# Performance work log

Measured on AMD Instinct MI355X. Metric: run time of the kernel, lower is better.

The kernel has to match this reference:

```python
import jax, jax.numpy as jnp
import numpy as np

B, N, D, DEPTH = 1, 512, 128, 4


def mlp_apply(W, x):
    # W: (depth, d, d), x: (..., d). First layer has no activation, then silu before each matmul.
    x = x @ W[0]
    for i in range(1, DEPTH):
        x = jax.nn.silu(x) @ W[i]
    return x


def _binop(x, y):
    # linear recurrence combine: s_t = a_t * s_{t-1} + b_t
    a1, b1 = x
    a2, b2 = y
    return (a1 * a2, a2 * b1 + b2)


def setup_inputs() -> dict:
    key = jax.random.key(0)
    ks = jax.random.split(key, 7)
    s = 0.02  # scale for projection weights (torch Linear-like init magnitude)
    return {
        "seq": jax.random.normal(ks[0], (B, N, D), jnp.float32),
        "W_mem": jax.random.normal(ks[1], (DEPTH, D, D), jnp.float32) * (D ** -0.5),
        "W_q": jax.random.normal(ks[2], (D, D), jnp.float32) * s,
        "W_kv": jax.random.normal(ks[3], (D, 2 * D), jnp.float32) * s,
        "W_mom": jax.random.normal(ks[4], (D, 1), jnp.float32) * s,
        "W_step": jax.random.normal(ks[5], (D, 1), jnp.float32) * s,
        "W_decay": jax.random.normal(ks[6], (D, 1), jnp.float32) * s,
    }


def reference(seq, W_mem, W_q, W_kv, W_mom, W_step, W_decay):
    b, n, d = seq.shape
    # --- store_memories ---
    adaptive_lr = (seq @ W_step)[..., 0]            # (b, n)
    adaptive_mom = seq @ W_mom                      # (b, n, 1)
    decay = jax.nn.sigmoid(seq @ W_decay)           # (b, n, 1)

    kv = seq.reshape(b * n, d) @ W_kv               # (bn, 2d)
    keys, values = kv[:, :d], kv[:, d:]

    def loss_fn(W, k, v):
        pred = mlp_apply(W, k)                      # (d,)
        # (pred - v)^2 .mean(-1).sum() for a single sample == mean over d
        return jnp.mean((pred - v) ** 2)

    # per-sample meta-gradients wrt memory MLP weights
    losses, grads = jax.vmap(jax.value_and_grad(loss_fn, argnums=0), in_axes=(None, 0, 0))(W_mem, keys, values)
    grads = grads.reshape(b, n, DEPTH, d, d)
    surprise = grads * (-adaptive_lr)[..., None, None, None]   # (b,n,depth,d,d)

    # momentum_t = adaptive_mom_t * momentum_{t-1} + surprise_t  (assoc. scan over n)
    am = adaptive_mom[..., None, None]              # (b, n, 1, 1, 1)
    _, momentum = jax.lax.associative_scan(_binop, (am, surprise), axis=1)

    # update_t = (1 - decay_t) * update_{t-1} + momentum_t
    dec = (1.0 - decay)[..., None, None]            # (b, n, 1, 1, 1)
    _, updates = jax.lax.associative_scan(_binop, (dec, momentum), axis=1)

    # --- retrieve_memories with per-token updated weights ---
    q = (seq @ W_q).reshape(b * n, d)
    W_tok = (W_mem[None, None] + updates).reshape(b * n, DEPTH, d, d)
    retrieved = jax.vmap(mlp_apply)(W_tok, q).reshape(b, n, d)
    return retrieved
```

## Files before the change

### kernel.cpp

```cpp
#include <hip/hip_runtime.h>
#include <hip/hip_bf16.h>
#include <math.h>

#define N 512
#define NN (N*N)
#define D 128
#define DD (D*D)
#define ND (N*D)
#define LSTR 132
#define CSTR 68

__device__ __forceinline__ float sigmoidf_(float x) { return 1.f / (1.f + expf(-x)); }

__global__ void k_transpose(const float* __restrict__ W_mem, float* __restrict__ WT) {
    int idx = blockIdx.x * 256 + threadIdx.x;
    int l = idx / DD;
    int r = idx % DD;
    int i = r / D;
    int j = r % D;
    WT[idx] = W_mem[(l + 1) * DD + j * D + i];
}

__global__ __launch_bounds__(512) void k_phase1(
    const float* __restrict__ seq, const float* __restrict__ W_mem,
    const float* __restrict__ W_q, const float* __restrict__ W_kv,
    const float* __restrict__ W_mom, const float* __restrict__ W_step,
    const float* __restrict__ W_decay, const float* __restrict__ WT,
    float* __restrict__ Q, float* __restrict__ INS, float* __restrict__ ES,
    float* __restrict__ am, float* __restrict__ dec)
{
    __shared__ float s_seq[2][D];
    __shared__ float s_bufA[2][D];
    __shared__ float s_bufB[2][D];
    __shared__ float s_p3[4][2][3][D];
    __shared__ float s_part[4][2][D];
    __shared__ float s_red8[8][3];
    __shared__ float s_lr[2];

    const int tid = threadIdx.x;
    const int p   = tid >> 7;
    const int j   = tid & 127;
    const int t0  = blockIdx.x * 2;
    const int i0  = p * 32;

    if (p < 2) s_seq[p][j] = seq[(t0 + p) * D + j];
    __syncthreads();

    {
        const int wv   = tid >> 6;
        const int tok  = wv >> 2;
        const int half = (wv >> 1) & 1;
        float sv = s_seq[tok][j];
        float p0 = 0.f, p1 = 0.f, p2 = 0.f;
        if (half == 0) { p0 = sv * W_step[j]; p1 = sv * W_mom[j]; }
        else           { p2 = sv * W_decay[j]; }
#pragma unroll
        for (int off = 32; off > 0; off >>= 1) {
            p0 += __shfl_down(p0, off);
            p1 += __shfl_down(p1, off);
            p2 += __shfl_down(p2, off);
        }
        if ((tid & 63) == 0) {
            s_red8[wv][0] = p0; s_red8[wv][1] = p1; s_red8[wv][2] = p2;
        }
    }
    __syncthreads();
    if (tid < 2) {
        int b = tid * 4;
        s_lr[tid]  = s_red8[b][0] + s_red8[b + 1][0];
        am[t0+tid] = s_red8[b][1] + s_red8[b + 1][1];
        dec[t0+tid]= 1.f - sigmoidf_(s_red8[b + 2][2] + s_red8[b + 3][2]);
    }

    float k0 = 0.f, v0 = 0.f, q0 = 0.f;
    float k1 = 0.f, v1 = 0.f, q1 = 0.f;
#pragma unroll 8
    for (int ii = 0; ii < 32; ii++) {
        int i = i0 + ii;
        float wk = W_kv[i * 256 + j];
        float wq = W_q[i * 128 + j];
        float wvv = W_kv[i * 256 + 128 + j];
        float a0 = s_seq[0][i], a1 = s_seq[1][i];
        k0 += a0 * wk;  k1 += a1 * wk;
        v0 += a0 * wvv; v1 += a1 * wvv;
        q0 += a0 * wq;  q1 += a1 * wq;
    }
    s_p3[p][0][0][j] = k0; s_p3[p][0][1][j] = v0; s_p3[p][0][2][j] = q0;
    s_p3[p][1][0][j] = k1; s_p3[p][1][1][j] = v1; s_p3[p][1][2][j] = q1;
    __syncthreads();

    float vj = 0.f;
    if (p < 2) {
        const int tok = p;
        float kj = s_p3[0][tok][0][j] + s_p3[1][tok][0][j] + s_p3[2][tok][0][j] + s_p3[3][tok][0][j];
        vj       = s_p3[0][tok][1][j] + s_p3[1][tok][1][j] + s_p3[2][tok][1][j] + s_p3[3][tok][1][j];
        float qj = s_p3[0][tok][2][j] + s_p3[1][tok][2][j] + s_p3[2][tok][2][j] + s_p3[3][tok][2][j];
        Q[(t0 + tok) * D + j] = qj;
        INS[(t0 + tok) * D + j] = kj;
        s_bufA[tok][j] = kj;
    }
    __syncthreads();

    float hreg[4];
    float pred = 0.f;
    {
        float (*bufs[2])[D] = { s_bufA, s_bufB };
        for (int l = 0; l < 4; l++) {
            float (*cur)[D] = bufs[l & 1];
            float (*nxt)[D] = bufs[(l + 1) & 1];
            const float* Wp = W_mem + l * DD + j;
            float a0 = 0.f, a1 = 0.f;
#pragma unroll 8
            for (int ii = 0; ii < 32; ii++) {
                int i = i0 + ii;
                float w = Wp[i * D];
                a0 += cur[0][i] * w;
                a1 += cur[1][i] * w;
            }
            s_part[p][0][j] = a0;
            s_part[p][1][j] = a1;
            __syncthreads();
            if (p < 2) {
                const int tok = p;
                float y = (s_part[0][tok][j] + s_part[1][tok][j])
                        + (s_part[2][tok][j] + s_part[3][tok][j]);
                hreg[l] = y;
                if (l < 3) {
                    float a = y * sigmoidf_(y);
                    nxt[tok][j] = a;
                    INS[(l + 1) * ND + (t0 + tok) * D + j] = a;
                } else {
                    pred = y;
                }
            }
            __syncthreads();
        }

        if (p < 2) {
            const int tok = p;
            float e = -s_lr[tok] * (2.f / (float)D) * (pred - vj);
            ES[3 * ND + (t0 + tok) * D + j] = e;
            bufs[0][tok][j] = e;
        }
        __syncthreads();

        for (int l = 3; l >= 1; l--) {
            float (*cur)[D] = bufs[(3 - l) & 1];
            float (*nxt)[D] = bufs[(3 - l + 1) & 1];
            const float* Wp = WT + (l - 1) * DD + j;
            float a0 = 0.f, a1 = 0.f;
#pragma unroll 8
            for (int ii = 0; ii < 32; ii++) {
                int i = i0 + ii;
                float w = Wp[i * D];
                a0 += cur[0][i] * w;
                a1 += cur[1][i] * w;
            }
            s_part[p][0][j] = a0;
            s_part[p][1][j] = a1;
            __syncthreads();
            if (p < 2) {
                const int tok = p;
                float g = (s_part[0][tok][j] + s_part[1][tok][j])
                        + (s_part[2][tok][j] + s_part[3][tok][j]);
                float h = hreg[l - 1];
                float sg = sigmoidf_(h);
                float e2 = g * (sg * (1.f + h * (1.f - sg)));
                ES[(l - 1) * ND + (t0 + tok) * D + j] = e2;
                nxt[tok][j] = e2;
            }
            __syncthreads();
        }
    }
}

__global__ __launch_bounds__(512) void k_logscan(
    const float* __restrict__ am, const float* __restrict__ dec,
    double* __restrict__ LA, double* __restrict__ LDp, int* __restrict__ NC)
{
    __shared__ double sa[N], sd[N];
    __shared__ int sn[N];
    const int t = threadIdx.x;
    float a = am[t];
    float d = dec[t];
    sa[t] = log((double)fmaxf(fabsf(a), 1e-38f));
    sd[t] = log((double)fmaxf(d, 1e-38f));
    sn[t] = (a < 0.f) ? 1 : 0;
    __syncthreads();
    for (int off = 1; off < N; off <<= 1) {
        double va = 0.0, vd = 0.0; int vn = 0;
        if (t >= off) { va = sa[t - off]; vd = sd[t - off]; vn = sn[t - off]; }
        __syncthreads();
        sa[t] += va; sd[t] += vd; sn[t] += vn;
        __syncthreads();
    }
    LA[t] = sa[t]; LDp[t] = sd[t]; NC[t] = sn[t];
}

__global__ __launch_bounds__(256) void k_build(
    const double* __restrict__ LA, const double* __restrict__ LDp,
    const int* __restrict__ NC,
    float* __restrict__ Amat, float* __restrict__ Dmat)
{
    int idx = blockIdx.x * 256 + threadIdx.x;
    int u = idx >> 9;
    int s = idx & (N - 1);
    float va = 0.f, vd = 0.f;
    if (s <= u) {
        va = expf((float)(LA[u] - LA[s]));
        if ((NC[u] - NC[s]) & 1) va = -va;
        vd = expf((float)(LDp[u] - LDp[s]));
    }
    Amat[idx] = va;
    Dmat[idx] = vd;
}

__global__ __launch_bounds__(256) void k_betamm(
    const float* __restrict__ Dmat, const float* __restrict__ Amat,
    float* __restrict__ betaP)
{
    const int bs = blockIdx.x;
    const int bt = blockIdx.y;
    const int z  = blockIdx.z;
    if (bs > bt) return;
    const int span = bt - bs + 1;
    const int chunk = (span + 3) >> 2;
    const int kBeg = bs + z * chunk;
    const int kEnd = (kBeg + chunk < bt + 1) ? (kBeg + chunk) : (bt + 1);
    if (kBeg >= kEnd) return;

    __shared__ float sA[32 * 34];
    __shared__ float sDT[32 * 34];

    const int tid = threadIdx.x;
    const int tx = tid & 15;
    const int ty = tid >> 4;
    float acc00 = 0.f, acc01 = 0.f, acc10 = 0.f, acc11 = 0.f;

    for (int kt = kBeg; kt < kEnd; kt++) {
        for (int i = tid; i < 1024; i += 256) {
            int r = i >> 5, c = i & 31;
            sA[r * 34 + c]  = Amat[(kt * 32 + r) * N + bs * 32 + c];
            sDT[c * 34 + r] = Dmat[(bt * 32 + r) * N + kt * 32 + c];
        }
        __syncthreads();
#pragma unroll 8
        for (int k = 0; k < 32; k++) {
            float2 a = *(float2*)&sA[k * 34 + 2 * tx];
            float2 d = *(float2*)&sDT[k * 34 + 2 * ty];
            acc00 += d.x * a.x; acc01 += d.x * a.y;
            acc10 += d.y * a.x; acc11 += d.y * a.y;
        }
        __syncthreads();
    }
    float* bp = betaP + z * NN + (bt * 32 + 2 * ty) * N + bs * 32 + 2 * tx;
    *(float2*)bp       = make_float2(acc00, acc01);
    *(float2*)(bp + N) = make_float2(acc10, acc11);
}

__global__ __launch_bounds__(256) void k_betared(
    const float* __restrict__ betaP, float* __restrict__ beta)
{
    int idx4 = blockIdx.x * 256 + threadIdx.x;
    int t  = idx4 >> 7;
    int s0 = (idx4 & 127) * 4;
    int bt = t >> 5, bs = s0 >> 5;
    float4 v = make_float4(0.f, 0.f, 0.f, 0.f);
    if (bs <= bt) {
        int span = bt - bs + 1;
        int chunk = (span + 3) >> 2;
        int nz = (span + chunk - 1) / chunk;
        v = *(const float4*)(betaP + t * N + s0);
        for (int z = 1; z < nz; z++) {
            float4 u = *(const float4*)(betaP + z * NN + t * N + s0);
            v.x += u.x; v.y += u.y; v.z += u.z; v.w += u.w;
        }
    }
    *(float4*)(beta + t * N + s0) = v;
}

__global__ __launch_bounds__(256) void k_layer(
    const float* __restrict__ Xsrc, float* __restrict__ Pout,
    const float* __restrict__ Wl, const float* __restrict__ INSl,
    const float* __restrict__ ESl, const float* __restrict__ beta,
    int mode)
{
    const int r = blockIdx.x;
    const int z = blockIdx.y;
    const bool isW = (z == 8);
    if (!isW && 4 * z > r) return;
    const int t0 = r * 16;
    const int lane = threadIdx.x;

    __shared__ __align__(16) float sX[16 * LSTR];
    __shared__ __align__(16) float sI[64 * LSTR];
    __shared__ __align__(16) float sE[32 * LSTR];
    __shared__ __align__(16) float sc[16 * CSTR];

    const int nzs = (r >> 2) + 1;
#pragma unroll
    for (int i = 0; i < 2; i++) {
        int f4 = lane + 256 * i;
        int row = f4 >> 5, c4 = f4 & 31;
        float4 v = ((const float4*)(Xsrc + t0 * D))[f4];
        if (mode) {
            for (int zz = 1; zz < nzs; zz++) {
                float4 u = ((const float4*)(Xsrc + zz * ND + t0 * D))[f4];
                v.x += u.x; v.y += u.y; v.z += u.z; v.w += u.w;
            }
            float4 w = ((const float4*)(Xsrc + 8 * ND + t0 * D))[f4];
            v.x += w.x; v.y += w.y; v.z += w.z; v.w += w.w;
            v.x = v.x * sigmoidf_(v.x); v.y = v.y * sigmoidf_(v.y);
            v.z = v.z * sigmoidf_(v.z); v.w = v.w * sigmoidf_(v.w);
        }
        *(float4*)(sX + row * LSTR + c4 * 4) = v;
    }

    if (isW) {
        __syncthreads();
        const int ti  = lane >> 4;
        const int j8  = (lane & 15) * 8;
        float acc[8];
#pragma unroll
        for (int b = 0; b < 8; b++) acc[b] = 0.f;
#pragma unroll 4
        for (int k = 0; k < D; k++) {
            float4 w0 = *(const float4*)(Wl + k * D + j8);
            float4 w1 = *(const float4*)(Wl + k * D + j8 + 4);
            float xv = sX[ti * LSTR + k];
            acc[0] += xv * w0.x; acc[1] += xv * w0.y;
            acc[2] += xv * w0.z; acc[3] += xv * w0.w;
            acc[4] += xv * w1.x; acc[5] += xv * w1.y;
            acc[6] += xv * w1.z; acc[7] += xv * w1.w;
        }
        float* yp = Pout + 8 * ND + (t0 + ti) * D + j8;
        *(float4*)yp       = make_float4(acc[0], acc[1], acc[2], acc[3]);
        *(float4*)(yp + 4) = make_float4(acc[4], acc[5], acc[6], acc[7]);
        return;
    }

    const int s0 = z * 64;
#pragma unroll
    for (int i = 0; i < 8; i++) {
        int f4 = lane + 256 * i;
        int row = f4 >> 5, c4 = f4 & 31;
        float4 a = ((const float4*)(INSl + s0 * D))[f4];
        *(float4*)(sI + row * LSTR + c4 * 4) = a;
    }

    const int rp = lane >> 5;
    const int sp = lane & 31;
    float b00 = beta[(t0 + 2 * rp) * N + s0 + sp];
    float b01 = beta[(t0 + 2 * rp) * N + s0 + sp + 32];
    float b10 = beta[(t0 + 2 * rp + 1) * N + s0 + sp];
    float b11 = beta[(t0 + 2 * rp + 1) * N + s0 + sp + 32];
    __syncthreads();

    float g00 = 0.f, g01 = 0.f, g10 = 0.f, g11 = 0.f;
#pragma unroll 8
    for (int k4 = 0; k4 < D; k4 += 4) {
        float4 a0 = *(float4*)(sX + (2 * rp) * LSTR + k4);
        float4 a1 = *(float4*)(sX + (2 * rp + 1) * LSTR + k4);
        float4 p0 = *(float4*)(sI + sp * LSTR + k4);
        float4 p1 = *(float4*)(sI + (sp + 32) * LSTR + k4);
        g00 += a0.x * p0.x + a0.y * p0.y + a0.z * p0.z + a0.w * p0.w;
        g01 += a0.x * p1.x + a0.y * p1.y + a0.z * p1.z + a0.w * p1.w;
        g10 += a1.x * p0.x + a1.y * p0.y + a1.z * p0.z + a1.w * p0.w;
        g11 += a1.x * p1.x + a1.y * p1.y + a1.z * p1.z + a1.w * p1.w;
    }
    sc[(2 * rp) * CSTR + sp]          = g00 * b00;
    sc[(2 * rp) * CSTR + sp + 32]     = g01 * b01;
    sc[(2 * rp + 1) * CSTR + sp]      = g10 * b10;
    sc[(2 * rp + 1) * CSTR + sp + 32] = g11 * b11;

    const int tp = lane >> 5;
    const int jc = (lane & 31) * 4;
    float acc[2][4];
#pragma unroll
    for (int a = 0; a < 2; a++)
#pragma unroll
        for (int b = 0; b < 4; b++) acc[a][b] = 0.f;

    for (int sub = 0; sub < 2; sub++) {
        __syncthreads();
#pragma unroll
        for (int i = 0; i < 4; i++) {
            int f4 = lane + 256 * i;
            int row = f4 >> 5, c4 = f4 & 31;
            float4 b = ((const float4*)(ESl + (s0 + sub * 32) * D))[f4];
            *(float4*)(sE + row * LSTR + c4 * 4) = b;
        }
        __syncthreads();
        const float* scp0 = sc + tp * CSTR + sub * 32;
        const float* scp1 = sc + (tp + 8) * CSTR + sub * 32;
#pragma unroll 8
        for (int s = 0; s < 32; s++) {
            float c0 = scp0[s];
            float c1 = scp1[s];
            float4 e = *(float4*)(sE + s * LSTR + jc);
            acc[0][0] += c0 * e.x; acc[0][1] += c0 * e.y;
            acc[0][2] += c0 * e.z; acc[0][3] += c0 * e.w;
            acc[1][0] += c1 * e.x; acc[1][1] += c1 * e.y;
            acc[1][2] += c1 * e.z; acc[1][3] += c1 * e.w;
        }
    }

    float* yp0 = Pout + z * ND + (t0 + tp) * D + jc;
    float* yp1 = Pout + z * ND + (t0 + tp + 8) * D + jc;
    *(float4*)yp0 = make_float4(acc[0][0], acc[0][1], acc[0][2], acc[0][3]);
    *(float4*)yp1 = make_float4(acc[1][0], acc[1][1], acc[1][2], acc[1][3]);
}

__global__ __launch_bounds__(256) void k_reduce(
    const float* __restrict__ P, float* __restrict__ out)
{
    int f4 = blockIdx.x * 256 + threadIdx.x;
    int t = f4 >> 5;
    int r = t >> 4;
    int nzs = (r >> 2) + 1;
    float4 v = ((const float4*)P)[f4];
    for (int zz = 1; zz < nzs; zz++) {
        float4 u = ((const float4*)(P + zz * ND))[f4];
        v.x += u.x; v.y += u.y; v.z += u.z; v.w += u.w;
    }
    float4 w = ((const float4*)(P + 8 * ND))[f4];
    v.x += w.x; v.y += w.y; v.z += w.z; v.w += w.w;
    ((float4*)out)[f4] = v;
}

extern "C" void kernel_launch(void* const* d_in, const int* in_sizes, int n_in,
                              void* d_out, int out_size, void* d_ws, size_t ws_size,
                              hipStream_t stream) {
    const float* seq     = (const float*)d_in[0];
    const float* W_mem   = (const float*)d_in[1];
    const float* W_q     = (const float*)d_in[2];
    const float* W_kv    = (const float*)d_in[3];
    const float* W_mom   = (const float*)d_in[4];
    const float* W_step  = (const float*)d_in[5];
    const float* W_decay = (const float*)d_in[6];
    float* out = (float*)d_out;

    float* ws   = (float*)d_ws;
    float* am   = ws;
    float* dec  = am + N;
    float* Q    = dec + N;
    float* INS  = Q + ND;
    float* ES   = INS + 4 * ND;
    float* beta = ES + 4 * ND;
    float* WT   = beta + NN;
    float* Amat = WT + 3 * DD;
    float* Dmat = Amat + NN;
    float* Pa   = Dmat + NN;
    float* Pb   = Pa + 9 * ND;
    double* LA  = (double*)(Pb + 9 * ND);
    double* LDp = LA + N;
    int* NC     = (int*)(LDp + N);
    float* betaP = Pa;

    k_transpose<<<192, 256, 0, stream>>>(W_mem, WT);
    k_phase1<<<N / 2, 512, 0, stream>>>(seq, W_mem, W_q, W_kv, W_mom, W_step, W_decay,
                                        WT, Q, INS, ES, am, dec);
    k_logscan<<<1, N, 0, stream>>>(am, dec, LA, LDp, NC);
    k_build<<<(NN) / 256, 256, 0, stream>>>(LA, LDp, NC, Amat, Dmat);
    dim3 mmgrid(N / 32, N / 32, 4);
    k_betamm<<<mmgrid, 256, 0, stream>>>(Dmat, Amat, betaP);
    k_betared<<<NN / 4 / 256, 256, 0, stream>>>(betaP, beta);

    dim3 lgrid(32, 9);
    k_layer<<<lgrid, 256, 0, stream>>>(Q,  Pa, W_mem,          INS,          ES,          beta, 0);
    k_layer<<<lgrid, 256, 0, stream>>>(Pa, Pb, W_mem + DD,     INS + ND,     ES + ND,     beta, 1);
    k_layer<<<lgrid, 256, 0, stream>>>(Pb, Pa, W_mem + 2 * DD, INS + 2 * ND, ES + 2 * ND, beta, 1);
    k_layer<<<lgrid, 256, 0, stream>>>(Pa, Pb, W_mem + 3 * DD, INS + 3 * ND, ES + 3 * ND, beta, 1);
    k_reduce<<<64, 256, 0, stream>>>(Pb, out);
}
```

Before: 163.5 us.

## Fuse decay-matrix construction into beta matmul and fold split-K reduction into layers

Removes the k_build kernel by computing the A and D decay-matrix tiles on the fly inside k_betamm from the log-scan prefix sums. It also removes the k_betared kernel: each k_layer reads the split-K partials directly and sums them per element. Partials now get their own workspace region so they survive across the layer kernels. This saves two launches and the NN-sized intermediate writes and reads. In exchange, expf is recomputed per tile load and each layer does repeated strided partial reads, four times over.

```diff
diff --git a/kernel.cpp b/kernel.cpp
--- a/kernel.cpp
+++ b/kernel.cpp
@@ -197,27 +197,9 @@
     LA[t] = sa[t]; LDp[t] = sd[t]; NC[t] = sn[t];
 }
 
-__global__ __launch_bounds__(256) void k_build(
+__global__ __launch_bounds__(256) void k_betamm(
     const double* __restrict__ LA, const double* __restrict__ LDp,
-    const int* __restrict__ NC,
-    float* __restrict__ Amat, float* __restrict__ Dmat)
-{
-    int idx = blockIdx.x * 256 + threadIdx.x;
-    int u = idx >> 9;
-    int s = idx & (N - 1);
-    float va = 0.f, vd = 0.f;
-    if (s <= u) {
-        va = expf((float)(LA[u] - LA[s]));
-        if ((NC[u] - NC[s]) & 1) va = -va;
-        vd = expf((float)(LDp[u] - LDp[s]));
-    }
-    Amat[idx] = va;
-    Dmat[idx] = vd;
-}
-
-__global__ __launch_bounds__(256) void k_betamm(
-    const float* __restrict__ Dmat, const float* __restrict__ Amat,
-    float* __restrict__ betaP)
+    const int* __restrict__ NC, float* __restrict__ betaP)
 {
     const int bs = blockIdx.x;
     const int bt = blockIdx.y;
@@ -240,8 +222,15 @@
     for (int kt = kBeg; kt < kEnd; kt++) {
         for (int i = tid; i < 1024; i += 256) {
             int r = i >> 5, c = i & 31;
-            sA[r * 34 + c]  = Amat[(kt * 32 + r) * N + bs * 32 + c];
-            sDT[c * 34 + r] = Dmat[(bt * 32 + r) * N + kt * 32 + c];
+            int u2 = kt * 32 + r, s2 = bs * 32 + c;
+            float va = 0.f;
+            if (s2 <= u2) {
+                va = expf((float)(LA[u2] - LA[s2]));
+                if ((NC[u2] - NC[s2]) & 1) va = -va;
+            }
+            sA[r * 34 + c] = va;
+            int u1 = bt * 32 + r, s1 = kt * 32 + c;
+            sDT[c * 34 + r] = (s1 <= u1) ? expf((float)(LDp[u1] - LDp[s1])) : 0.f;
         }
         __syncthreads();
 #pragma unroll 8
@@ -258,31 +247,21 @@
     *(float2*)(bp + N) = make_float2(acc10, acc11);
 }
 
-__global__ __launch_bounds__(256) void k_betared(
-    const float* __restrict__ betaP, float* __restrict__ beta)
-{
-    int idx4 = blockIdx.x * 256 + threadIdx.x;
-    int t  = idx4 >> 7;
-    int s0 = (idx4 & 127) * 4;
-    int bt = t >> 5, bs = s0 >> 5;
-    float4 v = make_float4(0.f, 0.f, 0.f, 0.f);
-    if (bs <= bt) {
-        int span = bt - bs + 1;
-        int chunk = (span + 3) >> 2;
-        int nz = (span + chunk - 1) / chunk;
-        v = *(const float4*)(betaP + t * N + s0);
-        for (int z = 1; z < nz; z++) {
-            float4 u = *(const float4*)(betaP + z * NN + t * N + s0);
-            v.x += u.x; v.y += u.y; v.z += u.z; v.w += u.w;
-        }
-    }
-    *(float4*)(beta + t * N + s0) = v;
+__device__ __forceinline__ float beta_at(const float* __restrict__ betaP, int t, int s) {
+    int bt = t >> 5, bs = s >> 5;
+    if (bs > bt) return 0.f;
+    int span = bt - bs + 1;
+    int chunk = (span + 3) >> 2;
+    int nz = (span + chunk - 1) / chunk;
+    float v = betaP[t * N + s];
+    for (int z = 1; z < nz; z++) v += betaP[z * NN + t * N + s];
+    return v;
 }
 
 __global__ __launch_bounds__(256) void k_layer(
     const float* __restrict__ Xsrc, float* __restrict__ Pout,
     const float* __restrict__ Wl, const float* __restrict__ INSl,
-    const float* __restrict__ ESl, const float* __restrict__ beta,
+    const float* __restrict__ ESl, const float* __restrict__ betaP,
     int mode)
 {
     const int r = blockIdx.x;
@@ -350,10 +329,10 @@
 
     const int rp = lane >> 5;
     const int sp = lane & 31;
-    float b00 = beta[(t0 + 2 * rp) * N + s0 + sp];
-    float b01 = beta[(t0 + 2 * rp) * N + s0 + sp + 32];
-    float b10 = beta[(t0 + 2 * rp + 1) * N + s0 + sp];
-    float b11 = beta[(t0 + 2 * rp + 1) * N + s0 + sp + 32];
+    float b00 = beta_at(betaP, t0 + 2 * rp,     s0 + sp);
+    float b01 = beta_at(betaP, t0 + 2 * rp,     s0 + sp + 32);
+    float b10 = beta_at(betaP, t0 + 2 * rp + 1, s0 + sp);
+    float b11 = beta_at(betaP, t0 + 2 * rp + 1, s0 + sp + 32);
     __syncthreads();
 
     float g00 = 0.f, g01 = 0.f, g10 = 0.f, g11 = 0.f;
@@ -440,36 +419,31 @@
     const float* W_decay = (const float*)d_in[6];
     float* out = (float*)d_out;
 
-    float* ws   = (float*)d_ws;
-    float* am   = ws;
-    float* dec  = am + N;
-    float* Q    = dec + N;
-    float* INS  = Q + ND;
-    float* ES   = INS + 4 * ND;
-    float* beta = ES + 4 * ND;
-    float* WT   = beta + NN;
-    float* Amat = WT + 3 * DD;
-    float* Dmat = Amat + NN;
-    float* Pa   = Dmat + NN;
-    float* Pb   = Pa + 9 * ND;
-    double* LA  = (double*)(Pb + 9 * ND);
-    double* LDp = LA + N;
-    int* NC     = (int*)(LDp + N);
-    float* betaP = Pa;
+    float* ws    = (float*)d_ws;
+    float* am    = ws;
+    float* dec   = am + N;
+    float* Q     = dec + N;
+    float* INS   = Q + ND;
+    float* ES    = INS + 4 * ND;
+    float* betaP = ES + 4 * ND;
+    float* Pa    = betaP + 4 * NN;
+    float* Pb    = Pa + 9 * ND;
+    float* WT    = Pb + 9 * ND;
+    double* LA   = (double*)(WT + 3 * DD);
+    double* LDp  = LA + N;
+    int* NC      = (int*)(LDp + N);
 
     k_transpose<<<192, 256, 0, stream>>>(W_mem, WT);
     k_phase1<<<N / 2, 512, 0, stream>>>(seq, W_mem, W_q, W_kv, W_mom, W_step, W_decay,
                                         WT, Q, INS, ES, am, dec);
     k_logscan<<<1, N, 0, stream>>>(am, dec, LA, LDp, NC);
-    k_build<<<(NN) / 256, 256, 0, stream>>>(LA, LDp, NC, Amat, Dmat);
     dim3 mmgrid(N / 32, N / 32, 4);
-    k_betamm<<<mmgrid, 256, 0, stream>>>(Dmat, Amat, betaP);
-    k_betared<<<NN / 4 / 256, 256, 0, stream>>>(betaP, beta);
+    k_betamm<<<mmgrid, 256, 0, stream>>>(LA, LDp, NC, betaP);
 
     dim3 lgrid(32, 9);
-    k_layer<<<lgrid, 256, 0, stream>>>(Q,  Pa, W_mem,          INS,          ES,          beta, 0);
-    k_layer<<<lgrid, 256, 0, stream>>>(Pa, Pb, W_mem + DD,     INS + ND,     ES + ND,     beta, 1);
-    k_layer<<<lgrid, 256, 0, stream>>>(Pb, Pa, W_mem + 2 * DD, INS + 2 * ND, ES + 2 * ND, beta, 1);
-    k_layer<<<lgrid, 256, 0, stream>>>(Pa, Pb, W_mem + 3 * DD, INS + 3 * ND, ES + 3 * ND, beta, 1);
+    k_layer<<<lgrid, 256, 0, stream>>>(Q,  Pa, W_mem,          INS,          ES,          betaP, 0);
+    k_layer<<<lgrid, 256, 0, stream>>>(Pa, Pb, W_mem + DD,     INS + ND,     ES + ND,     betaP, 1);
+    k_layer<<<lgrid, 256, 0, stream>>>(Pb, Pa, W_mem + 2 * DD, INS + 2 * ND, ES + 2 * ND, betaP, 1);
+    k_layer<<<lgrid, 256, 0, stream>>>(Pa, Pb, W_mem + 3 * DD, INS + 3 * ND, ES + 3 * ND, betaP, 1);
     k_reduce<<<64, 256, 0, stream>>>(Pb, out);
 }
```

New measurement: 163.5 us. Within noise of the previous version (+0.0%).
